# Kernel tuning notes

Measured on AMD Instinct MI355X. Metric: run time of the kernel, lower is better.

The kernel has to match this reference:

```python
import jax, jax.numpy as jnp
import numpy as np

V, BLOCK, L, H, D = 50257, 2048, 4, 8, 512
HD = D // H
FF = 4 * D
B, S = 2, 2048
EPS = 1e-5


def setup_inputs() -> dict:
    key = jax.random.key(0)
    ks = jax.random.split(key, 20)
    s = 0.02
    inp = {
        'idx': jax.random.randint(ks[0], (B, S), 0, V),
        'wte': jax.random.normal(ks[1], (V, D), jnp.float32) * s,
        'wpe': jax.random.normal(ks[2], (BLOCK, D), jnp.float32) * s,
        'ln1_w': jnp.ones((L, D), jnp.float32),
        'ln1_b': jnp.zeros((L, D), jnp.float32),
        'Wqkv': jax.random.normal(ks[3], (L, D, 3 * D), jnp.float32) * s,
        'bqkv': jnp.zeros((L, 3 * D), jnp.float32),
        'Wproj': jax.random.normal(ks[4], (L, D, D), jnp.float32) * (s / np.sqrt(2 * L)),
        'bproj': jnp.zeros((L, D), jnp.float32),
        'ln2_w': jnp.ones((L, D), jnp.float32),
        'ln2_b': jnp.zeros((L, D), jnp.float32),
        'Wfc': jax.random.normal(ks[5], (L, D, FF), jnp.float32) * s,
        'bfc': jnp.zeros((L, FF), jnp.float32),
        'Wfc2': jax.random.normal(ks[6], (L, FF, D), jnp.float32) * (s / np.sqrt(2 * L)),
        'bfc2': jnp.zeros((L, D), jnp.float32),
        'lnf_w': jnp.ones((D,), jnp.float32),
        'lnf_b': jnp.zeros((D,), jnp.float32),
    }
    return inp


def _ln(x, w, b):
    m = jnp.mean(x, axis=-1, keepdims=True)
    v = jnp.var(x, axis=-1, keepdims=True)
    return (x - m) * jax.lax.rsqrt(v + EPS) * w + b


def reference(idx, wte, wpe, ln1_w, ln1_b, Wqkv, bqkv, Wproj, bproj,
              ln2_w, ln2_b, Wfc, bfc, Wfc2, bfc2, lnf_w, lnf_b):
    b, s = idx.shape
    x = wte[idx] + wpe[:s][None]  # [B,S,D]
    causal = jnp.tril(jnp.ones((s, s), bool))
    scale = 1.0 / np.sqrt(HD)
    for l in range(L):
        h = _ln(x, ln1_w[l], ln1_b[l])
        qkv = h @ Wqkv[l] + bqkv[l]  # [B,S,3D]
        q, k, v = jnp.split(qkv, 3, axis=-1)
        q = q.reshape(b, s, H, HD).transpose(0, 2, 1, 3)
        k = k.reshape(b, s, H, HD).transpose(0, 2, 1, 3)
        v = v.reshape(b, s, H, HD).transpose(0, 2, 1, 3)
        att = jnp.einsum('bhqd,bhkd->bhqk', q, k) * scale
        att = jnp.where(causal, att, -jnp.inf)
        att = jax.nn.softmax(att, axis=-1)
        o = jnp.einsum('bhqk,bhkd->bhqd', att, v)
        o = o.transpose(0, 2, 1, 3).reshape(b, s, D)
        x = x + o @ Wproj[l] + bproj[l]
        h = _ln(x, ln2_w[l], ln2_b[l])
        h = jax.nn.gelu(h @ Wfc[l] + bfc[l], approximate=False)
        x = x + h @ Wfc2[l] + bfc2[l]
    x = _ln(x, lnf_w, lnf_b)
    logits = x @ wte.T  # weight-tied lm_head
    return logits
```

## Files before the change

kernel.cpp:

```cpp
#include <hip/hip_runtime.h>
#include <cmath>

typedef unsigned short u16;
typedef short bf16x8 __attribute__((ext_vector_type(8)));
typedef float f32x4 __attribute__((ext_vector_type(4)));
typedef unsigned short u16x8 __attribute__((ext_vector_type(8)));

#define VSZ 50257
#define DM 512
#define NL 4
#define NH 8
#define HDIM 64
#define FFD 2048
#define BB 2
#define SS 2048
#define RR (BB*SS)
#define LNEPS 1e-5f

__device__ __forceinline__ u16 f2bf(float f) {
  unsigned u = __float_as_uint(f);
  unsigned r = u + 0x7FFFu + ((u >> 16) & 1u);
  return (u16)(r >> 16);
}

__global__ void k_convert(const float* __restrict__ in, u16* __restrict__ out, long n) {
  long i = ((long)blockIdx.x * 256 + threadIdx.x) * 8;
  if (i + 8 <= n) {
    float4 a = *(const float4*)(in + i);
    float4 b = *(const float4*)(in + i + 4);
    u16x8 v;
    v[0]=f2bf(a.x); v[1]=f2bf(a.y); v[2]=f2bf(a.z); v[3]=f2bf(a.w);
    v[4]=f2bf(b.x); v[5]=f2bf(b.y); v[6]=f2bf(b.z); v[7]=f2bf(b.w);
    *(u16x8*)(out + i) = v;
  }
}

__global__ void k_transpose_convert(const float* __restrict__ in0, u16* __restrict__ out0, int K, int N) {
  const float* in = in0 + (size_t)blockIdx.z * K * N;
  u16* out = out0 + (size_t)blockIdx.z * K * N;
  __shared__ float tile[32][33];
  int tx = threadIdx.x, ty = threadIdx.y;
  int n0 = blockIdx.x * 32, k0 = blockIdx.y * 32;
  #pragma unroll
  for (int i = 0; i < 4; i++)
    tile[ty + i*8][tx] = in[(size_t)(k0 + ty + i*8) * N + n0 + tx];
  __syncthreads();
  #pragma unroll
  for (int i = 0; i < 4; i++)
    out[(size_t)(n0 + ty + i*8) * K + k0 + tx] = f2bf(tile[tx][ty + i*8]);
}

__global__ void k_embed(const int* __restrict__ idx, const float* __restrict__ wte,
                        const float* __restrict__ wpe, float* __restrict__ x) {
  int r = blockIdx.x;
  int s = r & (SS - 1);
  int t = threadIdx.x;
  int tok = idx[r];
  float4 a = *(const float4*)(wte + (size_t)tok * DM + t*4);
  float4 b = *(const float4*)(wpe + (size_t)s * DM + t*4);
  a.x += b.x; a.y += b.y; a.z += b.z; a.w += b.w;
  *(float4*)(x + (size_t)r * DM + t*4) = a;
}

__global__ __launch_bounds__(256) void k_ln(const float* __restrict__ x, const float* __restrict__ w,
                                            const float* __restrict__ b, u16* __restrict__ out) {
  int wave = threadIdx.x >> 6;
  int lane = threadIdx.x & 63;
  int r = blockIdx.x * 4 + wave;
  const float* xr = x + (size_t)r * DM + lane*8;
  float v[8];
  float4 a = *(const float4*)xr;
  float4 c = *(const float4*)(xr + 4);
  v[0]=a.x;v[1]=a.y;v[2]=a.z;v[3]=a.w;v[4]=c.x;v[5]=c.y;v[6]=c.z;v[7]=c.w;
  float s = 0.f, sq = 0.f;
  #pragma unroll
  for (int i=0;i<8;i++){ s += v[i]; sq += v[i]*v[i]; }
  #pragma unroll
  for (int m=1;m<64;m<<=1){ s += __shfl_xor(s, m, 64); sq += __shfl_xor(sq, m, 64); }
  float mean = s * (1.0f/DM);
  float var = sq * (1.0f/DM) - mean*mean;
  float rs = rsqrtf(var + LNEPS);
  int c0 = lane*8;
  u16x8 o;
  #pragma unroll
  for (int i=0;i<8;i++){
    float y = (v[i]-mean)*rs*w[c0+i] + b[c0+i];
    o[i] = f2bf(y);
  }
  *(u16x8*)(out + (size_t)r*DM + c0) = o;
}

#define GM_BIAS 1
#define GM_GELU 2
#define GM_RES  4
#define GM_BF16 8

template<int MODE>
__global__ __launch_bounds__(256, 2) void k_gemm_bt(
    const u16* __restrict__ A,
    const u16* __restrict__ Bt,
    const float* __restrict__ bias,
    void* __restrict__ C,
    int M, int N, int K, int Nbt) {
  __shared__ u16 As[128*72];
  __shared__ u16 Bs[128*72];
  int t = threadIdx.x;
  int n0 = blockIdx.x * 128;
  int m0 = blockIdx.y * 128;
  int w = t >> 6;
  int lane = t & 63;
  int wm = (w >> 1) * 64, wn = (w & 1) * 64;
  int lam = lane & 15, quad = lane >> 4;

  f32x4 zero = {0.f, 0.f, 0.f, 0.f};
  f32x4 acc[4][4];
  #pragma unroll
  for (int i=0;i<4;i++)
    #pragma unroll
    for (int j=0;j<4;j++) acc[i][j] = zero;

  int KT = K >> 6;
  for (int kt = 0; kt < KT; kt++) {
    #pragma unroll
    for (int i = 0; i < 4; i++) {
      int idx = t + i*256;
      int row = idx >> 3, c8 = (idx & 7) * 8;
      uint4 av = *(const uint4*)(A + (size_t)(m0 + row) * K + kt*64 + c8);
      *(uint4*)&As[row*72 + c8] = av;
      int nr = n0 + row;
      uint4 bv = {0u,0u,0u,0u};
      if (nr < Nbt) bv = *(const uint4*)(Bt + (size_t)nr * K + kt*64 + c8);
      *(uint4*)&Bs[row*72 + c8] = bv;
    }
    __syncthreads();
    #pragma unroll
    for (int s = 0; s < 2; s++) {
      bf16x8 af[4], bfv[4];
      #pragma unroll
      for (int i=0;i<4;i++) af[i]  = *(const bf16x8*)&As[(wm + i*16 + lam)*72 + s*32 + quad*8];
      #pragma unroll
      for (int i=0;i<4;i++) bfv[i] = *(const bf16x8*)&Bs[(wn + i*16 + lam)*72 + s*32 + quad*8];
      #pragma unroll
      for (int i=0;i<4;i++)
        #pragma unroll
        for (int j=0;j<4;j++)
          acc[i][j] = __builtin_amdgcn_mfma_f32_16x16x32_bf16(af[i], bfv[j], acc[i][j], 0, 0, 0);
    }
    __syncthreads();
  }

  #pragma unroll
  for (int j=0;j<4;j++) {
    int col = n0 + wn + j*16 + lam;
    if (col < N) {
      float bs = (MODE & GM_BIAS) ? bias[col] : 0.0f;
      #pragma unroll
      for (int i=0;i<4;i++) {
        int rowb = m0 + wm + i*16 + quad*4;
        #pragma unroll
        for (int r=0;r<4;r++) {
          float v2 = acc[i][j][r] + bs;
          if (MODE & GM_GELU) v2 = 0.5f * v2 * (1.0f + erff(v2 * 0.70710678118f));
          size_t off = (size_t)(rowb + r) * N + col;
          if (MODE & GM_RES) {
            ((float*)C)[off] += v2;
          } else if (MODE & GM_BF16) {
            ((u16*)C)[off] = f2bf(v2);
          } else {
            ((float*)C)[off] = v2;
          }
        }
      }
    }
  }
}

__global__ __launch_bounds__(64) void k_attn(const u16* __restrict__ qkv, u16* __restrict__ o) {
  int qt = blockIdx.x;
  int bh = blockIdx.y;
  int b = bh >> 3, h = bh & 7;
  int lane = threadIdx.x;
  int lam = lane & 15, quad = lane >> 4;
  int qbase = qt * 16;
  size_t base = (size_t)b * SS;

  __shared__ u16 Vs[32*72];
  __shared__ float Ps[16*36];

  const u16* qrow = qkv + (base + qbase + lam) * 1536 + h*64 + quad*8;
  bf16x8 qf0 = *(const bf16x8*)(qrow);
  bf16x8 qf1 = *(const bf16x8*)(qrow + 32);

  f32x4 zero = {0.f,0.f,0.f,0.f};
  float Mx[4], Ls[4];
  f32x4 oacc[4];
  #pragma unroll
  for (int r=0;r<4;r++){ Mx[r] = -1e30f; Ls[r] = 0.f; }
  #pragma unroll
  for (int d=0;d<4;d++) oacc[d] = zero;

  int nkb = ((qbase + 15) >> 5) + 1;
  for (int kb = 0; kb < nkb; kb++) {
    int ks = kb * 32;
    f32x4 sacc[2] = {zero, zero};
    #pragma unroll
    for (int kt2 = 0; kt2 < 2; kt2++) {
      const u16* krow = qkv + (base + ks + kt2*16 + lam) * 1536 + 512 + h*64 + quad*8;
      bf16x8 kf0 = *(const bf16x8*)(krow);
      bf16x8 kf1 = *(const bf16x8*)(krow + 32);
      sacc[kt2] = __builtin_amdgcn_mfma_f32_16x16x32_bf16(qf0, kf0, sacc[kt2], 0,0,0);
      sacc[kt2] = __builtin_amdgcn_mfma_f32_16x16x32_bf16(qf1, kf1, sacc[kt2], 0,0,0);
    }
    {
      int vrow = lane >> 3, c8 = (lane & 7) * 8;
      #pragma unroll
      for (int i=0;i<4;i++) {
        uint4 vv = *(const uint4*)(qkv + (base + ks + vrow + i*8) * 1536 + 1024 + h*64 + c8);
        *(uint4*)&Vs[(vrow + i*8)*72 + c8] = vv;
      }
    }
    float P[2][4];
    #pragma unroll
    for (int r=0;r<4;r++) {
      int q = qbase + quad*4 + r;
      float s0 = sacc[0][r] * 0.125f;
      float s1 = sacc[1][r] * 0.125f;
      if (ks + lam > q)       s0 = -1e30f;
      if (ks + 16 + lam > q)  s1 = -1e30f;
      float mx = fmaxf(s0, s1);
      #pragma unroll
      for (int m2=1;m2<16;m2<<=1) mx = fmaxf(mx, __shfl_xor(mx, m2, 64));
      float mn = fmaxf(Mx[r], mx);
      float alpha = __expf(Mx[r] - mn);
      float p0 = __expf(s0 - mn);
      float p1 = __expf(s1 - mn);
      float ps = p0 + p1;
      #pragma unroll
      for (int m2=1;m2<16;m2<<=1) ps += __shfl_xor(ps, m2, 64);
      Ls[r] = Ls[r]*alpha + ps;
      Mx[r] = mn;
      P[0][r] = p0; P[1][r] = p1;
      #pragma unroll
      for (int d=0;d<4;d++) oacc[d][r] *= alpha;
    }
    #pragma unroll
    for (int kt2=0;kt2<2;kt2++)
      #pragma unroll
      for (int r=0;r<4;r++)
        Ps[(quad*4+r)*36 + kt2*16 + lam] = P[kt2][r];
    __syncthreads();
    bf16x8 pf;
    #pragma unroll
    for (int j=0;j<8;j++) pf[j] = (short)f2bf(Ps[lam*36 + quad*8 + j]);
    #pragma unroll
    for (int d=0;d<4;d++) {
      bf16x8 vf;
      #pragma unroll
      for (int j=0;j<8;j++) vf[j] = (short)Vs[(quad*8+j)*72 + d*16 + lam];
      oacc[d] = __builtin_amdgcn_mfma_f32_16x16x32_bf16(pf, vf, oacc[d], 0,0,0);
    }
    __syncthreads();
  }
  #pragma unroll
  for (int d=0;d<4;d++)
    #pragma unroll
    for (int r=0;r<4;r++) {
      float val = oacc[d][r] / Ls[r];
      o[(base + qbase + quad*4 + r) * DM + h*64 + d*16 + lam] = f2bf(val);
    }
}

extern "C" void kernel_launch(void* const* d_in, const int* in_sizes, int n_in,
                              void* d_out, int out_size, void* d_ws, size_t ws_size,
                              hipStream_t stream) {
  const int*   idx   = (const int*)d_in[0];
  const float* wte   = (const float*)d_in[1];
  const float* wpe   = (const float*)d_in[2];
  const float* ln1w  = (const float*)d_in[3];
  const float* ln1b  = (const float*)d_in[4];
  const float* Wqkv  = (const float*)d_in[5];
  const float* bqkv  = (const float*)d_in[6];
  const float* Wproj = (const float*)d_in[7];
  const float* bproj = (const float*)d_in[8];
  const float* ln2w  = (const float*)d_in[9];
  const float* ln2b  = (const float*)d_in[10];
  const float* Wfc   = (const float*)d_in[11];
  const float* bfc   = (const float*)d_in[12];
  const float* Wfc2  = (const float*)d_in[13];
  const float* bfc2  = (const float*)d_in[14];
  const float* lnfw  = (const float*)d_in[15];
  const float* lnfb  = (const float*)d_in[16];
  float* logits = (float*)d_out;

  char* ws = (char*)d_ws;
  auto alloc = [&](size_t bytes) { char* p = ws; ws += (bytes + 255) & ~(size_t)255; return p; };
  float* x    = (float*)alloc((size_t)RR*DM*4);
  u16* hbuf   = (u16*)alloc((size_t)RR*DM*2);
  u16* qkvb   = (u16*)alloc((size_t)RR*1536*2);
  u16* obuf   = (u16*)alloc((size_t)RR*DM*2);
  u16* ffbuf  = (u16*)alloc((size_t)RR*FFD*2);
  u16* wte_bf = (u16*)alloc((size_t)VSZ*DM*2);
  u16* WqkvT  = (u16*)alloc((size_t)NL*1536*DM*2);
  u16* WprojT = (u16*)alloc((size_t)NL*DM*DM*2);
  u16* WfcT   = (u16*)alloc((size_t)NL*FFD*DM*2);
  u16* Wfc2T  = (u16*)alloc((size_t)NL*DM*FFD*2);

  long nwte = (long)VSZ * DM;
  k_convert<<<(int)((nwte/8 + 255)/256), 256, 0, stream>>>(wte, wte_bf, nwte);
  k_transpose_convert<<<dim3(1536/32, DM/32, NL), dim3(32,8), 0, stream>>>(Wqkv, WqkvT, DM, 1536);
  k_transpose_convert<<<dim3(DM/32, DM/32, NL),  dim3(32,8), 0, stream>>>(Wproj, WprojT, DM, DM);
  k_transpose_convert<<<dim3(FFD/32, DM/32, NL), dim3(32,8), 0, stream>>>(Wfc, WfcT, DM, FFD);
  k_transpose_convert<<<dim3(DM/32, FFD/32, NL), dim3(32,8), 0, stream>>>(Wfc2, Wfc2T, FFD, DM);

  k_embed<<<RR, 128, 0, stream>>>(idx, wte, wpe, x);

  for (int l = 0; l < NL; l++) {
    k_ln<<<RR/4, 256, 0, stream>>>(x, ln1w + l*DM, ln1b + l*DM, hbuf);
    k_gemm_bt<GM_BIAS|GM_BF16><<<dim3(1536/128, RR/128), 256, 0, stream>>>(
        hbuf, WqkvT + (size_t)l*1536*DM, bqkv + l*1536, qkvb, RR, 1536, DM, 1536);
    k_attn<<<dim3(SS/16, BB*NH), 64, 0, stream>>>(qkvb, obuf);
    k_gemm_bt<GM_BIAS|GM_RES><<<dim3(DM/128, RR/128), 256, 0, stream>>>(
        obuf, WprojT + (size_t)l*DM*DM, bproj + l*DM, x, RR, DM, DM, DM);
    k_ln<<<RR/4, 256, 0, stream>>>(x, ln2w + l*DM, ln2b + l*DM, hbuf);
    k_gemm_bt<GM_BIAS|GM_GELU|GM_BF16><<<dim3(FFD/128, RR/128), 256, 0, stream>>>(
        hbuf, WfcT + (size_t)l*FFD*DM, bfc + l*FFD, ffbuf, RR, FFD, DM, FFD);
    k_gemm_bt<GM_BIAS|GM_RES><<<dim3(DM/128, RR/128), 256, 0, stream>>>(
        ffbuf, Wfc2T + (size_t)l*DM*FFD, bfc2 + l*DM, x, RR, DM, FFD, DM);
  }
  k_ln<<<RR/4, 256, 0, stream>>>(x, lnfw, lnfb, hbuf);
  k_gemm_bt<0><<<dim3((VSZ+127)/128, RR/128), 256, 0, stream>>>(
      hbuf, wte_bf, nullptr, logits, RR, VSZ, DM, VSZ);
}
```

Baseline: 2.600 ms.

## Use direct global-to-LDS loads and XCD-aware tile swizzle in GEMM

Replaces the register-staged global->LDS copies in the bf16 GEMM with global_load_lds 16-byte direct loads, dropping the padded LDS stride (72->64) because the direct load writes contiguous lanes. It also remaps block IDs so consecutive blocks on each of 8 XCDs cover nearby tiles in M-major order, aiming for better L2 reuse. Out-of-range B rows are clamped instead of zero-filled. Removing the padding can introduce LDS bank conflicts on the fragment reads.

```diff
diff --git a/kernel.cpp b/kernel.cpp
--- a/kernel.cpp
+++ b/kernel.cpp
@@ -21,6 +21,12 @@
   unsigned u = __float_as_uint(f);
   unsigned r = u + 0x7FFFu + ((u >> 16) & 1u);
   return (u16)(r >> 16);
+}
+
+__device__ __forceinline__ void gload16(const void* g, void* l) {
+  __builtin_amdgcn_global_load_lds(
+      (const __attribute__((address_space(1))) unsigned int*)g,
+      (__attribute__((address_space(3))) unsigned int*)l, 16, 0, 0);
 }
 
 __global__ void k_convert(const float* __restrict__ in, u16* __restrict__ out, long n) {
@@ -102,16 +108,40 @@
     const float* __restrict__ bias,
     void* __restrict__ C,
     int M, int N, int K, int Nbt) {
-  __shared__ u16 As[128*72];
-  __shared__ u16 Bs[128*72];
+  __shared__ u16 As[128*64];
+  __shared__ u16 Bs[128*64];
   int t = threadIdx.x;
-  int n0 = blockIdx.x * 128;
-  int m0 = blockIdx.y * 128;
+
+  unsigned gx = gridDim.x, gy = gridDim.y;
+  unsigned nwg = gx * gy;
+  unsigned bid = blockIdx.y * gx + blockIdx.x;
+  unsigned u = bid;
+  if ((nwg & 7u) == 0u) {
+    unsigned chunk = nwg >> 3;
+    u = (bid & 7u) * chunk + (bid >> 3);
+  }
+  unsigned mIdx = u % gy;
+  unsigned nIdx = u / gy;
+  int m0 = mIdx * 128, n0 = nIdx * 128;
+
   int w = t >> 6;
   int lane = t & 63;
   int wm = (w >> 1) * 64, wn = (w & 1) * 64;
   int lam = lane & 15, quad = lane >> 4;
 
+  int srow = t >> 3;
+  int scol = (t & 7) * 8;
+  const u16* gA = A + (size_t)(m0 + srow) * K + scol;
+  const u16* gB[4];
+  #pragma unroll
+  for (int i = 0; i < 4; i++) {
+    int nr = n0 + srow + i*32;
+    if (nr >= Nbt) nr = Nbt - 1;
+    gB[i] = Bt + (size_t)nr * K + scol;
+  }
+  u16* lA = &As[(size_t)t * 8];
+  u16* lB = &Bs[(size_t)t * 8];
+
   f32x4 zero = {0.f, 0.f, 0.f, 0.f};
   f32x4 acc[4][4];
   #pragma unroll
@@ -121,25 +151,20 @@
 
   int KT = K >> 6;
   for (int kt = 0; kt < KT; kt++) {
+    int ko = kt * 64;
     #pragma unroll
     for (int i = 0; i < 4; i++) {
-      int idx = t + i*256;
-      int row = idx >> 3, c8 = (idx & 7) * 8;
-      uint4 av = *(const uint4*)(A + (size_t)(m0 + row) * K + kt*64 + c8);
-      *(uint4*)&As[row*72 + c8] = av;
-      int nr = n0 + row;
-      uint4 bv = {0u,0u,0u,0u};
-      if (nr < Nbt) bv = *(const uint4*)(Bt + (size_t)nr * K + kt*64 + c8);
-      *(uint4*)&Bs[row*72 + c8] = bv;
+      gload16(gA + (size_t)i*32*K + ko, lA + i*256*8);
+      gload16(gB[i] + ko,              lB + i*256*8);
     }
     __syncthreads();
     #pragma unroll
     for (int s = 0; s < 2; s++) {
       bf16x8 af[4], bfv[4];
       #pragma unroll
-      for (int i=0;i<4;i++) af[i]  = *(const bf16x8*)&As[(wm + i*16 + lam)*72 + s*32 + quad*8];
-      #pragma unroll
-      for (int i=0;i<4;i++) bfv[i] = *(const bf16x8*)&Bs[(wn + i*16 + lam)*72 + s*32 + quad*8];
+      for (int i=0;i<4;i++) af[i]  = *(const bf16x8*)&As[(wm + i*16 + lam)*64 + s*32 + quad*8];
+      #pragma unroll
+      for (int i=0;i<4;i++) bfv[i] = *(const bf16x8*)&Bs[(wn + i*16 + lam)*64 + s*32 + quad*8];
       #pragma unroll
       for (int i=0;i<4;i++)
         #pragma unroll
```

After: 2.319 ms. -10.8%, faster.
